# Performance work log

Hardware: AMD Instinct MI355X
Metric: run time of the kernel (lower is better)

The kernel has to match this reference:

```python
import jax, jax.numpy as jnp
import numpy as np

NC_MEM = 64          # nTemporalMemoryChannels
NC_IMG = 64          # nImageFeatureChannels
FTL_RATIO = 0.5      # temporalFTLRatio
N_BLOCKS = 3         # nTemporalBlocks
B, H, W = 32, 64, 96
M = 32               # memory buffer length (= max(memory_idx)+1)


def setup_inputs() -> dict:
    key = jax.random.key(0)
    ks = jax.random.split(key, 8)
    eye = jnp.eye(4, dtype=jnp.float32)
    img_features = jax.random.normal(ks[0], (B, NC_IMG, H, W), jnp.float32)
    prev_mem_features = jax.random.normal(ks[1], (M, NC_MEM, H, W), jnp.float32)
    # extrinsics: random perturbation around identity so torch.inverse-equivalent is well conditioned
    prev_extrinsics = 0.1 * jax.random.normal(ks[2], (M, 4, 4), jnp.float32) + eye
    cur_extrinsics = 0.1 * jax.random.normal(ks[3], (B, 4, 4), jnp.float32) + eye
    memory_idx = jnp.arange(B, dtype=jnp.int32)
    use_memory = jax.random.randint(ks[4], (B,), 0, 2).astype(bool)
    NC = NC_MEM + NC_IMG
    Ws = jax.random.normal(ks[5], (N_BLOCKS, NC, NC), jnp.float32) * (1.0 / np.sqrt(NC))
    bs = jax.random.normal(ks[6], (N_BLOCKS, NC), jnp.float32) * 0.01
    return {
        "img_features": img_features,
        "prev_mem_features": prev_mem_features,
        "prev_extrinsics": prev_extrinsics,
        "cur_extrinsics": cur_extrinsics,
        "memory_idx": memory_idx,
        "use_memory": use_memory,
        "Ws": Ws,
        "bs": bs,
    }


def _apply_ftl(xf, feats, ratio):
    # Feature Transform Layer: first `ratio` fraction of channels (rounded down
    # to a multiple of 4) treated as groups of homogeneous 4-vectors per pixel,
    # warped by the 4x4 transform xf; remaining channels pass through.
    b, c, h, w = feats.shape
    nc_ftl = (int(c * ratio) // 4) * 4
    g = nc_ftl // 4
    pts = feats[:, :nc_ftl].reshape(b, g, 4, h * w)
    pts = jnp.einsum("bij,bgjp->bgip", xf, pts).reshape(b, nc_ftl, h, w)
    return jnp.concatenate([pts, feats[:, nc_ftl:]], axis=1)


def reference(img_features, prev_mem_features, prev_extrinsics, cur_extrinsics,
              memory_idx, use_memory, Ws, bs):
    eye = jnp.eye(4, dtype=prev_extrinsics.dtype)
    # --- transform_memory_features (gather + extrinsics warp, masked) ---
    mem_g = prev_mem_features[memory_idx]              # [B, NC_MEM, H, W]
    prev_ext_g = prev_extrinsics[memory_idx]           # [B, 4, 4]
    # entries with use_memory=False are zeroed; guard inverse with identity
    safe_prev = jnp.where(use_memory[:, None, None], prev_ext_g, eye)
    prev_cam0_to_world = jnp.linalg.inv(safe_prev)
    xf = jnp.einsum("bij,bjk->bik", cur_extrinsics, prev_cam0_to_world)
    mem_xfed = _apply_ftl(xf, mem_g, FTL_RATIO)
    mem_xfed = jnp.where(use_memory[:, None, None, None], mem_xfed,
                         jnp.zeros((), mem_xfed.dtype))
    # --- forward_one_step: concat + 1x1 conv stack (pointwise matmuls) ---
    x = jnp.concatenate([mem_xfed, img_features], axis=1)  # [B, 128, H, W]
    n = Ws.shape[0]
    for i in range(n):
        x = jnp.einsum("oc,bchw->bohw", Ws[i], x) + bs[i][None, :, None, None]
        if i != n - 1:
            x = jax.nn.relu(x)
    fused_features = x[:, NC_MEM:]                     # returned output
    return fused_features
```

## Files before the change

### kernel.cpp

```cpp
#include <hip/hip_runtime.h>
#include <hip/hip_fp16.h>

#define NC_MEM 64
#define NC_IMG 64
#define NC     128
#define B_     32
#define H_     64
#define W_     96
#define HW_    (H_ * W_)
#define P_TILE 128
#define NTILES (HW_ / P_TILE)
#define FS     520
#define FOFF(pt, ks) ((((pt) * 4) + (ks)) * FS)

#define WA_HI  0
#define WA_LO  98304
#define XF_OFF 196608
#define UM_OFF 198656

typedef _Float16 f16x8 __attribute__((ext_vector_type(8)));
typedef __attribute__((ext_vector_type(4))) float f32x4;

__device__ inline unsigned pk2h(float a, float b) {
    __half2 h = __floats2half2_rn(a, b);
    return *(const unsigned*)&h;
}

__global__ void prep(const float* __restrict__ Ws,
                     const float* __restrict__ prev_ext,
                     const float* __restrict__ cur_ext,
                     const int* __restrict__ mem_idx,
                     const unsigned char* __restrict__ um_raw,
                     unsigned char* __restrict__ wsb) {
    if (blockIdx.x < 192) {
        int idx = blockIdx.x * 256 + threadIdx.x;
        int l = idx >> 14, r = idx & 16383, o = r >> 7, c = r & 127;
        float w = Ws[idx];
        __half hi = __float2half_rn(w);
        __half lo = __float2half_rn(w - __half2float(hi));
        int mt = o >> 4, lm = o & 15, ks = c >> 5, kr = c & 31, q = kr >> 3, j = kr & 7;
        int lane = q * 16 + lm;
        int di = ((((l * 8 + mt) * 4 + ks) * 64 + lane) << 3) + j;
        ((unsigned short*)(wsb + WA_HI))[di] = __half_as_ushort(hi);
        ((unsigned short*)(wsb + WA_LO))[di] = __half_as_ushort(lo);
        return;
    }
    int tb = threadIdx.x;
    if (tb >= 64) return;
    bool flag = (tb < 32) && (tb & 3) && (um_raw[tb] != 0);
    bool is_bool = __any(flag);
    if (tb >= B_) return;
    int b = tb;
    bool um = is_bool ? (um_raw[b] != 0) : (((const int*)um_raw)[b] != 0);
    int mi = mem_idx[b];

    float a[16];
#pragma unroll
    for (int i = 0; i < 16; ++i)
        a[i] = um ? prev_ext[mi * 16 + i] : ((i % 5 == 0) ? 1.f : 0.f);

    float s0 = a[0]*a[5]  - a[1]*a[4];
    float s1 = a[0]*a[6]  - a[2]*a[4];
    float s2 = a[0]*a[7]  - a[3]*a[4];
    float s3 = a[1]*a[6]  - a[2]*a[5];
    float s4 = a[1]*a[7]  - a[3]*a[5];
    float s5 = a[2]*a[7]  - a[3]*a[6];
    float c5 = a[10]*a[15] - a[11]*a[14];
    float c4 = a[9]*a[15]  - a[11]*a[13];
    float c3 = a[9]*a[14]  - a[10]*a[13];
    float c2 = a[8]*a[15]  - a[11]*a[12];
    float c1 = a[8]*a[14]  - a[10]*a[12];
    float c0 = a[8]*a[13]  - a[9]*a[12];
    float det = s0*c5 - s1*c4 + s2*c3 + s3*c2 - s4*c1 + s5*c0;
    float id = 1.0f / det;

    float inv[16];
    inv[0]  = ( a[5]*c5  - a[6]*c4  + a[7]*c3)  * id;
    inv[1]  = (-a[1]*c5  + a[2]*c4  - a[3]*c3)  * id;
    inv[2]  = ( a[13]*s5 - a[14]*s4 + a[15]*s3) * id;
    inv[3]  = (-a[9]*s5  + a[10]*s4 - a[11]*s3) * id;
    inv[4]  = (-a[4]*c5  + a[6]*c2  - a[7]*c1)  * id;
    inv[5]  = ( a[0]*c5  - a[2]*c2  + a[3]*c1)  * id;
    inv[6]  = (-a[12]*s5 + a[14]*s2 - a[15]*s1) * id;
    inv[7]  = ( a[8]*s5  - a[10]*s2 + a[11]*s1) * id;
    inv[8]  = ( a[4]*c4  - a[5]*c2  + a[7]*c0)  * id;
    inv[9]  = (-a[0]*c4  + a[1]*c2  - a[3]*c0)  * id;
    inv[10] = ( a[12]*s4 - a[13]*s2 + a[15]*s0) * id;
    inv[11] = (-a[8]*s4  + a[9]*s2  - a[11]*s0) * id;
    inv[12] = (-a[4]*c3  + a[5]*c1  - a[6]*c0)  * id;
    inv[13] = ( a[0]*c3  - a[1]*c1  + a[2]*c0)  * id;
    inv[14] = (-a[12]*s3 + a[13]*s1 - a[14]*s0) * id;
    inv[15] = ( a[8]*s3  - a[9]*s1  + a[10]*s0) * id;

    float* xf = (float*)(wsb + XF_OFF) + b * 16;
#pragma unroll
    for (int i = 0; i < 4; ++i)
#pragma unroll
        for (int j2 = 0; j2 < 4; ++j2) {
            float s = 0.f;
#pragma unroll
            for (int k = 0; k < 4; ++k)
                s += cur_ext[b * 16 + i * 4 + k] * inv[k * 4 + j2];
            xf[i * 4 + j2] = s;
        }
    ((float*)(wsb + UM_OFF))[b] = um ? 1.f : 0.f;
}

__global__ __launch_bounds__(512, 4)
void fused_main(const float* __restrict__ img, const float* __restrict__ mem,
                const int* __restrict__ mem_idx, const float* __restrict__ bs,
                const unsigned char* __restrict__ wsb, float* __restrict__ out) {
    __shared__ unsigned short xh[2][32 * FS];

    const int t   = threadIdx.x;
    const int b   = blockIdx.y;
    const int hw0 = blockIdx.x * P_TILE;
    const bool umb = ((const float*)(wsb + UM_OFF))[b] != 0.f;
    const int mi  = mem_idx[b];

    const f16x8* __restrict__ WH = (const f16x8*)(wsb + WA_HI);
    const f16x8* __restrict__ WL = (const f16x8*)(wsb + WA_LO);

    const int w    = t >> 6;
    const int lane = t & 63;
    const int wq   = lane >> 4;
    const int lm   = lane & 15;
    const int mt0  = 2 * (w & 3);
    const int nt0  = 4 * (w >> 2);

#define FI(l, mt, ks) (((((l) * 8 + (mt)) * 4) + (ks)) * 64 + lane)

    {
        const int q   = t & 31;
        const int og  = t >> 5;
        const int px0 = hw0 + q * 4;
        if (umb) {
            const int c0 = og * 8;
            const float* basep = (c0 < NC_MEM)
                ? (mem + ((size_t)mi * NC_MEM + c0) * HW_ + px0)
                : (img + ((size_t)b * NC_IMG + (c0 - NC_MEM)) * HW_ + px0);
            f32x4 v[8];
#pragma unroll
            for (int cc = 0; cc < 8; ++cc)
                v[cc] = *(const f32x4*)(basep + (size_t)cc * HW_);
            if (og < 4) {
                float xfv[16];
                const float* xfp = (const float*)(wsb + XF_OFF) + b * 16;
#pragma unroll
                for (int j = 0; j < 4; ++j)
                    *(f32x4*)&xfv[j * 4] = *(const f32x4*)&xfp[j * 4];
#pragma unroll
                for (int sg = 0; sg < 2; ++sg) {
#pragma unroll
                    for (int i = 0; i < 4; ++i) {
                        float a0 = v[4*sg+0][i], a1 = v[4*sg+1][i];
                        float a2 = v[4*sg+2][i], a3 = v[4*sg+3][i];
                        v[4*sg+0][i] = xfv[0]*a0  + xfv[1]*a1  + xfv[2]*a2  + xfv[3]*a3;
                        v[4*sg+1][i] = xfv[4]*a0  + xfv[5]*a1  + xfv[6]*a2  + xfv[7]*a3;
                        v[4*sg+2][i] = xfv[8]*a0  + xfv[9]*a1  + xfv[10]*a2 + xfv[11]*a3;
                        v[4*sg+3][i] = xfv[12]*a0 + xfv[13]*a1 + xfv[14]*a2 + xfv[15]*a3;
                    }
                }
            }
            const int bus = FOFF(q >> 2, og >> 2) + ((og & 3) * 16 + (q & 3) * 4) * 8;
#pragma unroll
            for (int i = 0; i < 4; ++i) {
                uint4 pk;
                pk.x = pk2h(v[0][i], v[1][i]);
                pk.y = pk2h(v[2][i], v[3][i]);
                pk.z = pk2h(v[4][i], v[5][i]);
                pk.w = pk2h(v[6][i], v[7][i]);
                *(uint4*)&xh[0][bus + i * 8] = pk;
            }
        } else {
            const int gg = 16 + og;
            const int c0 = gg * 4 - NC_MEM;
            f32x4 u[4];
#pragma unroll
            for (int cc = 0; cc < 4; ++cc)
                u[cc] = *(const f32x4*)(img + ((size_t)b * NC_IMG + c0 + cc) * HW_ + px0);
            const int bus = FOFF(q >> 2, gg >> 3)
                          + (((gg & 7) >> 1) * 16 + (q & 3) * 4) * 8 + (gg & 1) * 4;
#pragma unroll
            for (int i = 0; i < 4; ++i)
                *(uint2*)&xh[0][bus + i * 8] =
                    make_uint2(pk2h(u[0][i], u[1][i]), pk2h(u[2][i], u[3][i]));
        }
    }

    const int kpa = umb ? 0 : 2, kpb = umb ? 1 : 3;
    f16x8 p0h = WH[FI(0, mt0,     kpa)], p0l = WL[FI(0, mt0,     kpa)];
    f16x8 p1h = WH[FI(0, mt0 + 1, kpa)], p1l = WL[FI(0, mt0 + 1, kpa)];
    f16x8 p2h = WH[FI(0, mt0,     kpb)], p2l = WL[FI(0, mt0,     kpb)];
    f16x8 p3h = WH[FI(0, mt0 + 1, kpb)], p3l = WL[FI(0, mt0 + 1, kpb)];

    __syncthreads();

    const unsigned short* xr = xh[0];
    f32x4 acc[2][4];

    auto run_ks = [&](int ks, f16x8 ah0, f16x8 al0, f16x8 ah1, f16x8 al1) {
#pragma unroll
        for (int nt = 0; nt < 4; ++nt) {
            f16x8 bh = *(const f16x8*)&xr[FOFF(nt0 + nt, ks) + lane * 8];
            acc[0][nt] = __builtin_amdgcn_mfma_f32_16x16x32_f16(ah0, bh, acc[0][nt], 0, 0, 0);
            acc[1][nt] = __builtin_amdgcn_mfma_f32_16x16x32_f16(ah1, bh, acc[1][nt], 0, 0, 0);
            acc[0][nt] = __builtin_amdgcn_mfma_f32_16x16x32_f16(al0, bh, acc[0][nt], 0, 0, 0);
            acc[1][nt] = __builtin_amdgcn_mfma_f32_16x16x32_f16(al1, bh, acc[1][nt], 0, 0, 0);
        }
    };
    auto writeback = [&](unsigned short* xw) {
#pragma unroll
        for (int mi2 = 0; mi2 < 2; ++mi2) {
            const int mt = mt0 + mi2;
            const int ks2 = mt >> 1;
            const int lane_f = ((mt & 1) * 2 + (wq >> 1)) * 16 + lm;
            const int j0 = (wq & 1) * 4;
#pragma unroll
            for (int nt = 0; nt < 4; ++nt) {
                float v0 = fmaxf(acc[mi2][nt][0], 0.f);
                float v1 = fmaxf(acc[mi2][nt][1], 0.f);
                float v2 = fmaxf(acc[mi2][nt][2], 0.f);
                float v3 = fmaxf(acc[mi2][nt][3], 0.f);
                *(uint2*)&xw[FOFF(nt0 + nt, ks2) + lane_f * 8 + j0] =
                    make_uint2(pk2h(v0, v1), pk2h(v2, v3));
            }
        }
    };

#pragma unroll
    for (int mi2 = 0; mi2 < 2; ++mi2) {
        f32x4 bv = *(const f32x4*)&bs[0 * NC + (mt0 + mi2) * 16 + wq * 4];
#pragma unroll
        for (int nt = 0; nt < 4; ++nt) acc[mi2][nt] = bv;
    }
    __builtin_amdgcn_s_setprio(1);
    if (umb) {
        run_ks(0, p0h, p0l, p1h, p1l);
        run_ks(1, p2h, p2l, p3h, p3l);
        run_ks(2, WH[FI(0, mt0, 2)], WL[FI(0, mt0, 2)],
                  WH[FI(0, mt0 + 1, 2)], WL[FI(0, mt0 + 1, 2)]);
        run_ks(3, WH[FI(0, mt0, 3)], WL[FI(0, mt0, 3)],
                  WH[FI(0, mt0 + 1, 3)], WL[FI(0, mt0 + 1, 3)]);
    } else {
        run_ks(2, p0h, p0l, p1h, p1l);
        run_ks(3, p2h, p2l, p3h, p3l);
    }
    __builtin_amdgcn_s_setprio(0);
    f16x8 q0h = WH[FI(1, mt0, 0)],     q0l = WL[FI(1, mt0, 0)];
    f16x8 q1h = WH[FI(1, mt0 + 1, 0)], q1l = WL[FI(1, mt0 + 1, 0)];
    f16x8 q2h = WH[FI(1, mt0, 1)],     q2l = WL[FI(1, mt0, 1)];
    f16x8 q3h = WH[FI(1, mt0 + 1, 1)], q3l = WL[FI(1, mt0 + 1, 1)];
    writeback(xh[1]);
    __syncthreads();

    xr = xh[1];
#pragma unroll
    for (int mi2 = 0; mi2 < 2; ++mi2) {
        f32x4 bv = *(const f32x4*)&bs[1 * NC + (mt0 + mi2) * 16 + wq * 4];
#pragma unroll
        for (int nt = 0; nt < 4; ++nt) acc[mi2][nt] = bv;
    }
    __builtin_amdgcn_s_setprio(1);
    run_ks(0, q0h, q0l, q1h, q1l);
    run_ks(1, q2h, q2l, q3h, q3l);
    run_ks(2, WH[FI(1, mt0, 2)], WL[FI(1, mt0, 2)],
              WH[FI(1, mt0 + 1, 2)], WL[FI(1, mt0 + 1, 2)]);
    run_ks(3, WH[FI(1, mt0, 3)], WL[FI(1, mt0, 3)],
              WH[FI(1, mt0 + 1, 3)], WL[FI(1, mt0 + 1, 3)]);
    __builtin_amdgcn_s_setprio(0);
    const int mt2 = 4 + (w & 3);
    f16x8 r0h = WH[FI(2, mt2, 0)], r0l = WL[FI(2, mt2, 0)];
    f16x8 r1h = WH[FI(2, mt2, 1)], r1l = WL[FI(2, mt2, 1)];
    f16x8 r2h = WH[FI(2, mt2, 2)], r2l = WL[FI(2, mt2, 2)];
    f16x8 r3h = WH[FI(2, mt2, 3)], r3l = WL[FI(2, mt2, 3)];
    writeback(xh[0]);
    __syncthreads();

    {
        xr = xh[0];
        f32x4 a2[4];
        f32x4 bv = *(const f32x4*)&bs[2 * NC + mt2 * 16 + wq * 4];
#pragma unroll
        for (int nt = 0; nt < 4; ++nt) a2[nt] = bv;
        auto run2 = [&](int ks, f16x8 ah, f16x8 al) {
#pragma unroll
            for (int nt = 0; nt < 4; ++nt) {
                f16x8 bh = *(const f16x8*)&xr[FOFF(nt0 + nt, ks) + lane * 8];
                a2[nt] = __builtin_amdgcn_mfma_f32_16x16x32_f16(ah, bh, a2[nt], 0, 0, 0);
                a2[nt] = __builtin_amdgcn_mfma_f32_16x16x32_f16(al, bh, a2[nt], 0, 0, 0);
            }
        };
        __builtin_amdgcn_s_setprio(1);
        run2(0, r0h, r0l);
        run2(1, r1h, r1l);
        run2(2, r2h, r2l);
        run2(3, r3h, r3l);
        __builtin_amdgcn_s_setprio(0);
        const int oc0 = mt2 * 16 + wq * 4 - 64;
#pragma unroll
        for (int nt = 0; nt < 4; ++nt) {
            float* dst = out + ((size_t)b * 64 + oc0) * HW_ + hw0 + (nt0 + nt) * 16 + lm;
#pragma unroll
            for (int r = 0; r < 4; ++r)
                __builtin_nontemporal_store(a2[nt][r], dst + (size_t)r * HW_);
        }
    }
#undef FI
}

extern "C" void kernel_launch(void* const* d_in, const int* in_sizes, int n_in,
                              void* d_out, int out_size, void* d_ws, size_t ws_size,
                              hipStream_t stream) {
    const float* img  = (const float*)d_in[0];
    const float* mem  = (const float*)d_in[1];
    const float* pext = (const float*)d_in[2];
    const float* cext = (const float*)d_in[3];
    const int*   midx = (const int*)d_in[4];
    const unsigned char* umem = (const unsigned char*)d_in[5];
    const float* Ws   = (const float*)d_in[6];
    const float* bs   = (const float*)d_in[7];
    float* out = (float*)d_out;
    unsigned char* wsb = (unsigned char*)d_ws;

    hipLaunchKernelGGL(prep, dim3(193), dim3(256), 0, stream,
                       Ws, pext, cext, midx, umem, wsb);
    hipLaunchKernelGGL(fused_main, dim3(NTILES, B_), dim3(512), 0, stream,
                       img, mem, midx, bs, wsb, out);
}
```

Before: 162.2 us.

## Single-buffer LDS activations with rotated swizzle to double occupancy

Replaces the two LDS activation buffers with one buffer, adding an extra barrier before each layer's writeback so reads finish before overwriting. A per-pixel-tile rotation (XOFF) of the 8-half slot index is applied to writes and reads to change bank mapping, and launch bounds are raised to 8 blocks per CU. The goal is to halve LDS footprint so more workgroups fit per CU and latency is hidden better, at the cost of extra syncs and possibly tighter register limits causing spills.

```diff
diff --git a/kernel.cpp b/kernel.cpp
--- a/kernel.cpp
+++ b/kernel.cpp
@@ -12,6 +12,7 @@
 #define NTILES (HW_ / P_TILE)
 #define FS     520
 #define FOFF(pt, ks) ((((pt) * 4) + (ks)) * FS)
+#define XOFF(pt, ks, blk) (FOFF(pt, ks) + ((((blk) + (pt)) & 63) << 3))
 
 #define WA_HI  0
 #define WA_LO  98304
@@ -106,11 +107,11 @@
     ((float*)(wsb + UM_OFF))[b] = um ? 1.f : 0.f;
 }
 
-__global__ __launch_bounds__(512, 4)
+__global__ __launch_bounds__(512, 8)
 void fused_main(const float* __restrict__ img, const float* __restrict__ mem,
                 const int* __restrict__ mem_idx, const float* __restrict__ bs,
                 const unsigned char* __restrict__ wsb, float* __restrict__ out) {
-    __shared__ unsigned short xh[2][32 * FS];
+    __shared__ unsigned short xh[32 * FS];
 
     const int t   = threadIdx.x;
     const int b   = blockIdx.y;
@@ -134,6 +135,7 @@
         const int q   = t & 31;
         const int og  = t >> 5;
         const int px0 = hw0 + q * 4;
+        const int pt  = q >> 2;
         if (umb) {
             const int c0 = og * 8;
             const float* basep = (c0 < NC_MEM)
@@ -162,7 +164,7 @@
                     }
                 }
             }
-            const int bus = FOFF(q >> 2, og >> 2) + ((og & 3) * 16 + (q & 3) * 4) * 8;
+            const int bk0 = (og & 3) * 16 + (q & 3) * 4;
 #pragma unroll
             for (int i = 0; i < 4; ++i) {
                 uint4 pk;
@@ -170,7 +172,7 @@
                 pk.y = pk2h(v[2][i], v[3][i]);
                 pk.z = pk2h(v[4][i], v[5][i]);
                 pk.w = pk2h(v[6][i], v[7][i]);
-                *(uint4*)&xh[0][bus + i * 8] = pk;
+                *(uint4*)&xh[XOFF(pt, og >> 2, bk0 + i)] = pk;
             }
         } else {
             const int gg = 16 + og;
@@ -179,11 +181,11 @@
 #pragma unroll
             for (int cc = 0; cc < 4; ++cc)
                 u[cc] = *(const f32x4*)(img + ((size_t)b * NC_IMG + c0 + cc) * HW_ + px0);
-            const int bus = FOFF(q >> 2, gg >> 3)
-                          + (((gg & 7) >> 1) * 16 + (q & 3) * 4) * 8 + (gg & 1) * 4;
+            const int bk0 = ((gg & 7) >> 1) * 16 + (q & 3) * 4;
+            const int hoff = (gg & 1) * 4;
 #pragma unroll
             for (int i = 0; i < 4; ++i)
-                *(uint2*)&xh[0][bus + i * 8] =
+                *(uint2*)&xh[XOFF(pt, gg >> 3, bk0 + i) + hoff] =
                     make_uint2(pk2h(u[0][i], u[1][i]), pk2h(u[2][i], u[3][i]));
         }
     }
@@ -196,20 +198,19 @@
 
     __syncthreads();
 
-    const unsigned short* xr = xh[0];
     f32x4 acc[2][4];
 
     auto run_ks = [&](int ks, f16x8 ah0, f16x8 al0, f16x8 ah1, f16x8 al1) {
 #pragma unroll
         for (int nt = 0; nt < 4; ++nt) {
-            f16x8 bh = *(const f16x8*)&xr[FOFF(nt0 + nt, ks) + lane * 8];
+            f16x8 bh = *(const f16x8*)&xh[XOFF(nt0 + nt, ks, lane)];
             acc[0][nt] = __builtin_amdgcn_mfma_f32_16x16x32_f16(ah0, bh, acc[0][nt], 0, 0, 0);
             acc[1][nt] = __builtin_amdgcn_mfma_f32_16x16x32_f16(ah1, bh, acc[1][nt], 0, 0, 0);
             acc[0][nt] = __builtin_amdgcn_mfma_f32_16x16x32_f16(al0, bh, acc[0][nt], 0, 0, 0);
             acc[1][nt] = __builtin_amdgcn_mfma_f32_16x16x32_f16(al1, bh, acc[1][nt], 0, 0, 0);
         }
     };
-    auto writeback = [&](unsigned short* xw) {
+    auto writeback = [&]() {
 #pragma unroll
         for (int mi2 = 0; mi2 < 2; ++mi2) {
             const int mt = mt0 + mi2;
@@ -222,7 +223,7 @@
                 float v1 = fmaxf(acc[mi2][nt][1], 0.f);
                 float v2 = fmaxf(acc[mi2][nt][2], 0.f);
                 float v3 = fmaxf(acc[mi2][nt][3], 0.f);
-                *(uint2*)&xw[FOFF(nt0 + nt, ks2) + lane_f * 8 + j0] =
+                *(uint2*)&xh[XOFF(nt0 + nt, ks2, lane_f) + j0] =
                     make_uint2(pk2h(v0, v1), pk2h(v2, v3));
             }
         }
@@ -251,10 +252,10 @@
     f16x8 q1h = WH[FI(1, mt0 + 1, 0)], q1l = WL[FI(1, mt0 + 1, 0)];
     f16x8 q2h = WH[FI(1, mt0, 1)],     q2l = WL[FI(1, mt0, 1)];
     f16x8 q3h = WH[FI(1, mt0 + 1, 1)], q3l = WL[FI(1, mt0 + 1, 1)];
-    writeback(xh[1]);
-    __syncthreads();
-
-    xr = xh[1];
+    __syncthreads();
+    writeback();
+    __syncthreads();
+
 #pragma unroll
     for (int mi2 = 0; mi2 < 2; ++mi2) {
         f32x4 bv = *(const f32x4*)&bs[1 * NC + (mt0 + mi2) * 16 + wq * 4];
@@ -274,11 +275,11 @@
     f16x8 r1h = WH[FI(2, mt2, 1)], r1l = WL[FI(2, mt2, 1)];
     f16x8 r2h = WH[FI(2, mt2, 2)], r2l = WL[FI(2, mt2, 2)];
     f16x8 r3h = WH[FI(2, mt2, 3)], r3l = WL[FI(2, mt2, 3)];
-    writeback(xh[0]);
+    __syncthreads();
+    writeback();
     __syncthreads();
 
     {
-        xr = xh[0];
         f32x4 a2[4];
         f32x4 bv = *(const f32x4*)&bs[2 * NC + mt2 * 16 + wq * 4];
 #pragma unroll
@@ -286,7 +287,7 @@
         auto run2 = [&](int ks, f16x8 ah, f16x8 al) {
 #pragma unroll
             for (int nt = 0; nt < 4; ++nt) {
-                f16x8 bh = *(const f16x8*)&xr[FOFF(nt0 + nt, ks) + lane * 8];
+                f16x8 bh = *(const f16x8*)&xh[XOFF(nt0 + nt, ks, lane)];
                 a2[nt] = __builtin_amdgcn_mfma_f32_16x16x32_f16(ah, bh, a2[nt], 0, 0, 0);
                 a2[nt] = __builtin_amdgcn_mfma_f32_16x16x32_f16(al, bh, a2[nt], 0, 0, 0);
             }
```

Result: slower. 322.6 us (+98.9%).
